# Optimization experiments

Hardware: AMD Instinct MI355X
Metric: run time of the kernel (lower is better)

## Reference

```python
import jax, jax.numpy as jnp
import numpy as np

N_NODES = 20000
N_EDGES = 640000
N_FEATS = 3703
HIDDEN = 50
N_CLASSES = 6
N_KENN_LAYERS = 3
# clause: not C_c(x) OR C_c(y) OR not Cite(x,y)  -> literal signs
SIGNS = np.array([-1.0, 1.0, -1.0], dtype=np.float32)


def setup_inputs() -> dict:
    key = jax.random.key(0)
    ks = jax.random.split(key, 12)
    features = jax.random.normal(ks[0], (N_NODES, N_FEATS), dtype=jnp.float32)
    relations = jax.random.normal(ks[1], (N_EDGES, 1), dtype=jnp.float32)
    sx = jax.random.randint(ks[2], (N_EDGES,), 0, N_NODES)
    sy = jax.random.randint(ks[3], (N_EDGES,), 0, N_NODES)

    def dense(k, fan_in, fan_out):
        return jax.random.normal(k, (fan_in, fan_out), dtype=jnp.float32) / np.sqrt(fan_in).astype(np.float32)

    W1 = dense(ks[4], N_FEATS, HIDDEN); b1 = jnp.zeros((HIDDEN,), jnp.float32)
    W2 = dense(ks[5], HIDDEN, HIDDEN);  b2 = jnp.zeros((HIDDEN,), jnp.float32)
    W3 = dense(ks[6], HIDDEN, HIDDEN);  b3 = jnp.zeros((HIDDEN,), jnp.float32)
    W4 = dense(ks[7], HIDDEN, N_CLASSES); b4 = jnp.zeros((N_CLASSES,), jnp.float32)
    # one learnable clause weight per class-clause, per KENN layer (init 0.5 as in KENN)
    clause_weights = jnp.full((N_KENN_LAYERS, N_CLASSES), 0.5, dtype=jnp.float32)
    return dict(features=features, relations=relations, sx=sx, sy=sy,
                W1=W1, b1=b1, W2=W2, b2=b2, W3=W3, b3=b3, W4=W4, b4=b4,
                clause_weights=clause_weights)


def _kenn_layer(z, relations, sx, sy, cw):
    # z: [N, C]; relations: [E, 1]; cw: [C] clause weights
    n = z.shape[0]
    zx = z[sx]                                   # [E, C] gather head literals
    zy = z[sy]                                   # [E, C] gather tail literals
    rel = jnp.broadcast_to(relations, (relations.shape[0], z.shape[1]))  # [E, C]
    signs = jnp.asarray(SIGNS)
    # signed literal preactivations per clause: [E, C, 3]
    v = jnp.stack([-zx, zy, -rel], axis=-1)
    # KENN boost: delta = w_c * softmax(signed preacts) * sign
    d = cw[None, :, None] * jax.nn.softmax(v, axis=-1) * signs[None, None, :]
    # scatter unary deltas back to nodes (relation delta is discarded)
    dz = jax.ops.segment_sum(d[..., 0], sx, num_segments=n)
    dz = dz + jax.ops.segment_sum(d[..., 1], sy, num_segments=n)
    return z + dz


def reference(features, relations, sx, sy, W1, b1, W2, b2, W3, b3, W4, b4, clause_weights):
    # MLP preactivations (dropout inactive at inference)
    x = jax.nn.relu(features @ W1 + b1)
    x = jax.nn.relu(x @ W2 + b2)
    x = jax.nn.relu(x @ W3 + b3)
    z = x @ W4 + b4                               # [N, 6]
    for i in range(N_KENN_LAYERS):
        z = _kenn_layer(z, relations, sx, sy, clause_weights[i])
    return jax.nn.softmax(z, axis=-1)
```

## Files before the change

kernel.cpp:

```cpp
#include <hip/hip_runtime.h>

#define M_NODES 20000
#define K_FEATS 3703
#define PADK 3712
#define NH 50
#define NC 6
#define N_EDGES_C 640000
#define NKB 116

typedef __attribute__((ext_vector_type(8))) __bf16 bf16x8;
typedef __attribute__((ext_vector_type(4))) float f32x4;

__global__ void k_packB(const float* __restrict__ W1, unsigned short* __restrict__ Bh,
                        unsigned short* __restrict__ Bl) {
  int idx = blockIdx.x * 256 + threadIdx.x;
  if (idx >= NKB * 4 * 64 * 8) return;
  int j = idx & 7;
  int lane = (idx >> 3) & 63;
  int t = (idx >> 9) & 3;
  int kb = idx >> 11;
  int k = kb * 32 + (lane >> 4) * 8 + j;
  int c = t * 16 + (lane & 15);
  float v = (k < K_FEATS && c < NH) ? W1[k * NH + c] : 0.f;
  __bf16 hb = (__bf16)v;
  float hf = (float)hb;
  __bf16 lb = (__bf16)(v - hf);
  Bh[idx] = *(unsigned short*)&hb;
  Bl[idx] = *(unsigned short*)&lb;
}

__global__ __launch_bounds__(256) void k_gemm1(const float* __restrict__ A,
    const unsigned short* __restrict__ Bph, const unsigned short* __restrict__ Bpl,
    float* __restrict__ part, int KS) {
  const int lane = threadIdx.x & 63;
  const int w = threadIdx.x >> 6;
  const int row0 = blockIdx.x * 128 + w * 32;
  const int s = blockIdx.y;
  const int ks = s * KS;
  const int ke = (ks + KS < PADK) ? ks + KS : PADK;
  const int nsteps = (ke - ks) >> 5;
  const int g = lane >> 4;
  const int rl = lane & 15;
  const int r0c = min(row0 + rl, M_NODES - 1);
  const int r1c = min(row0 + 16 + rl, M_NODES - 1);
  const float* a0p = A + (size_t)r0c * K_FEATS + 8 * g;
  const float* a1p = A + (size_t)r1c * K_FEATS + 8 * g;
  const bf16x8* BH = (const bf16x8*)Bph;
  const bf16x8* BL = (const bf16x8*)Bpl;

  f32x4 acc[2][4];
  #pragma unroll
  for (int i = 0; i < 2; ++i)
    #pragma unroll
    for (int t = 0; t < 4; ++t) acc[i][t] = (f32x4){0.f, 0.f, 0.f, 0.f};

  #define LOADA(d0, d1, k0) {                                     \
    d0[0] = *(const float4*)(a0p + (k0));                         \
    d0[1] = *(const float4*)(a0p + (k0) + 4);                     \
    d1[0] = *(const float4*)(a1p + (k0));                         \
    d1[1] = *(const float4*)(a1p + (k0) + 4); }
  #define LOADAG(d0, d1, k0) {                                    \
    _Pragma("unroll") for (int j = 0; j < 8; ++j) {               \
      int gk = (k0) + 8 * g + j;                                  \
      float v0 = (gk < K_FEATS) ? a0p[(k0) + j] : 0.f;            \
      float v1 = (gk < K_FEATS) ? a1p[(k0) + j] : 0.f;            \
      ((float*)d0)[j] = v0; ((float*)d1)[j] = v1; } }
  #define LDSEL(d0, d1, k0) {                                     \
    if ((k0) + 32 > K_FEATS) { LOADAG(d0, d1, k0) }               \
    else { LOADA(d0, d1, k0) } }

  #define BODY(sa0, sa1, k0) {                                    \
    const int kb4 = ((k0) >> 5) * 4;                              \
    bf16x8 bh0 = BH[(kb4 + 0) * 64 + lane];                       \
    bf16x8 bh1 = BH[(kb4 + 1) * 64 + lane];                       \
    bf16x8 bh2 = BH[(kb4 + 2) * 64 + lane];                       \
    bf16x8 bh3 = BH[(kb4 + 3) * 64 + lane];                       \
    bf16x8 bl0 = BL[(kb4 + 0) * 64 + lane];                       \
    bf16x8 bl1 = BL[(kb4 + 1) * 64 + lane];                       \
    bf16x8 bl2 = BL[(kb4 + 2) * 64 + lane];                       \
    bf16x8 bl3 = BL[(kb4 + 3) * 64 + lane];                       \
    bf16x8 ah0, al0, ah1, al1;                                    \
    _Pragma("unroll") for (int j = 0; j < 8; ++j) {               \
      float xv = ((const float*)sa0)[j];                          \
      __bf16 hb = (__bf16)xv; float hf = (float)hb;               \
      ah0[j] = hb; al0[j] = (__bf16)(xv - hf);                    \
      float yv = ((const float*)sa1)[j];                          \
      __bf16 hb2 = (__bf16)yv; float hf2 = (float)hb2;            \
      ah1[j] = hb2; al1[j] = (__bf16)(yv - hf2);                  \
    }                                                             \
    acc[0][0] = __builtin_amdgcn_mfma_f32_16x16x32_bf16(ah0, bh0, acc[0][0], 0, 0, 0); \
    acc[0][1] = __builtin_amdgcn_mfma_f32_16x16x32_bf16(ah0, bh1, acc[0][1], 0, 0, 0); \
    acc[0][2] = __builtin_amdgcn_mfma_f32_16x16x32_bf16(ah0, bh2, acc[0][2], 0, 0, 0); \
    acc[0][3] = __builtin_amdgcn_mfma_f32_16x16x32_bf16(ah0, bh3, acc[0][3], 0, 0, 0); \
    acc[1][0] = __builtin_amdgcn_mfma_f32_16x16x32_bf16(ah1, bh0, acc[1][0], 0, 0, 0); \
    acc[1][1] = __builtin_amdgcn_mfma_f32_16x16x32_bf16(ah1, bh1, acc[1][1], 0, 0, 0); \
    acc[1][2] = __builtin_amdgcn_mfma_f32_16x16x32_bf16(ah1, bh2, acc[1][2], 0, 0, 0); \
    acc[1][3] = __builtin_amdgcn_mfma_f32_16x16x32_bf16(ah1, bh3, acc[1][3], 0, 0, 0); \
    acc[0][0] = __builtin_amdgcn_mfma_f32_16x16x32_bf16(al0, bh0, acc[0][0], 0, 0, 0); \
    acc[0][1] = __builtin_amdgcn_mfma_f32_16x16x32_bf16(al0, bh1, acc[0][1], 0, 0, 0); \
    acc[0][2] = __builtin_amdgcn_mfma_f32_16x16x32_bf16(al0, bh2, acc[0][2], 0, 0, 0); \
    acc[0][3] = __builtin_amdgcn_mfma_f32_16x16x32_bf16(al0, bh3, acc[0][3], 0, 0, 0); \
    acc[1][0] = __builtin_amdgcn_mfma_f32_16x16x32_bf16(al1, bh0, acc[1][0], 0, 0, 0); \
    acc[1][1] = __builtin_amdgcn_mfma_f32_16x16x32_bf16(al1, bh1, acc[1][1], 0, 0, 0); \
    acc[1][2] = __builtin_amdgcn_mfma_f32_16x16x32_bf16(al1, bh2, acc[1][2], 0, 0, 0); \
    acc[1][3] = __builtin_amdgcn_mfma_f32_16x16x32_bf16(al1, bh3, acc[1][3], 0, 0, 0); \
    acc[0][0] = __builtin_amdgcn_mfma_f32_16x16x32_bf16(ah0, bl0, acc[0][0], 0, 0, 0); \
    acc[0][1] = __builtin_amdgcn_mfma_f32_16x16x32_bf16(ah0, bl1, acc[0][1], 0, 0, 0); \
    acc[0][2] = __builtin_amdgcn_mfma_f32_16x16x32_bf16(ah0, bl2, acc[0][2], 0, 0, 0); \
    acc[0][3] = __builtin_amdgcn_mfma_f32_16x16x32_bf16(ah0, bl3, acc[0][3], 0, 0, 0); \
    acc[1][0] = __builtin_amdgcn_mfma_f32_16x16x32_bf16(ah1, bl0, acc[1][0], 0, 0, 0); \
    acc[1][1] = __builtin_amdgcn_mfma_f32_16x16x32_bf16(ah1, bl1, acc[1][1], 0, 0, 0); \
    acc[1][2] = __builtin_amdgcn_mfma_f32_16x16x32_bf16(ah1, bl2, acc[1][2], 0, 0, 0); \
    acc[1][3] = __builtin_amdgcn_mfma_f32_16x16x32_bf16(ah1, bl3, acc[1][3], 0, 0, 0); }

  float4 p0a[2], p0b[2], p1a[2], p1b[2], p2a[2], p2b[2];
  LDSEL(p0a, p0b, ks);
  if (nsteps > 1) LDSEL(p1a, p1b, ks + 32);
  if (nsteps > 2) LDSEL(p2a, p2b, ks + 64);

  int t = 0;
  for (; t + 3 <= nsteps; t += 3) {
    const int k0 = ks + (t << 5);
    BODY(p0a, p0b, k0);
    if (t + 3 < nsteps) LDSEL(p0a, p0b, k0 + 96);
    BODY(p1a, p1b, k0 + 32);
    if (t + 4 < nsteps) LDSEL(p1a, p1b, k0 + 128);
    BODY(p2a, p2b, k0 + 64);
    if (t + 5 < nsteps) LDSEL(p2a, p2b, k0 + 160);
  }
  if (t < nsteps)     BODY(p0a, p0b, ks + (t << 5));
  if (t + 1 < nsteps) BODY(p1a, p1b, ks + ((t + 1) << 5));
  #undef LOADA
  #undef LOADAG
  #undef LDSEL
  #undef BODY

  float* p = part + (size_t)s * 1000000;
  #pragma unroll
  for (int i = 0; i < 2; ++i) {
    #pragma unroll
    for (int t2 = 0; t2 < 4; ++t2) {
      int col = t2 * 16 + rl;
      if (col < NH) {
        int rowb = row0 + i * 16 + g * 4;
        f32x4 v = acc[i][t2];
        #pragma unroll
        for (int q = 0; q < 4; ++q) {
          int row = rowb + q;
          if (row < M_NODES) p[row * NH + col] = v[q];
        }
      }
    }
  }
}

__global__ void k_epi(const float* __restrict__ part, const float* __restrict__ b1,
                      float* __restrict__ x1, int S) {
  int i = blockIdx.x * 256 + threadIdx.x;
  if (i >= M_NODES * NH) return;
  float v = b1[i % NH];
  for (int s = 0; s < S; ++s) v += part[(size_t)s * 1000000 + i];
  x1[i] = fmaxf(v, 0.f);
}

__global__ __launch_bounds__(256) void k_mlp(const float* __restrict__ x1,
    const float* __restrict__ W2, const float* __restrict__ b2,
    const float* __restrict__ W3, const float* __restrict__ b3,
    const float* __restrict__ W4, const float* __restrict__ b4,
    float* __restrict__ z) {
  __shared__ float lX[32 * 51];
  __shared__ float lW2[50 * 52];
  __shared__ float lW3[50 * 52];
  __shared__ float lW4[50 * 8];
  const int tid = threadIdx.x;
  const int row0 = blockIdx.x * 32;
  for (int idx = tid; idx < 2500; idx += 256) {
    int k = idx / 50, n = idx % 50;
    lW2[k * 52 + n] = W2[idx];
    lW3[k * 52 + n] = W3[idx];
  }
  for (int idx = tid; idx < 300; idx += 256) {
    int k = idx / 6, n = idx % 6;
    lW4[k * 8 + n] = W4[idx];
  }
  for (int idx = tid; idx < 1600; idx += 256) {
    int r = idx / 50, k = idx % 50;
    int gr = row0 + r;
    lX[r * 51 + k] = (gr < M_NODES) ? x1[gr * 50 + k] : 0.f;
  }
  __syncthreads();
  const int r = tid >> 3, cg = tid & 7;
  float x[50];
  #pragma unroll
  for (int k = 0; k < 50; ++k) x[k] = lX[r * 51 + k];

  for (int layer = 0; layer < 2; ++layer) {
    const float* lW = (layer == 0) ? lW2 : lW3;
    const float* bg = (layer == 0) ? b2 : b3;
    float acc[7];
    #pragma unroll
    for (int j = 0; j < 7; ++j) {
      int n = cg + 8 * j;
      acc[j] = (n < 50) ? bg[n] : 0.f;
    }
    #pragma unroll
    for (int k = 0; k < 50; ++k) {
      float xk = x[k];
      #pragma unroll
      for (int j = 0; j < 7; ++j) {
        int n = cg + 8 * j;
        if (n < 50) acc[j] = fmaf(xk, lW[k * 52 + n], acc[j]);
      }
    }
    __syncthreads();
    #pragma unroll
    for (int j = 0; j < 7; ++j) {
      int n = cg + 8 * j;
      if (n < 50) lX[r * 51 + n] = fmaxf(acc[j], 0.f);
    }
    __syncthreads();
    #pragma unroll
    for (int k = 0; k < 50; ++k) x[k] = lX[r * 51 + k];
  }
  if (cg < 6) {
    float accz = b4[cg];
    #pragma unroll
    for (int k = 0; k < 50; ++k) accz = fmaf(x[k], lW4[k * 8 + cg], accz);
    int gr = row0 + r;
    if (gr < M_NODES) z[gr * 6 + cg] = accz;
  }
}

__global__ void k_count(const int* __restrict__ sx, const int* __restrict__ sy,
                        int* __restrict__ cnt) {
  int e = blockIdx.x * 256 + threadIdx.x;
  if (e >= N_EDGES_C) return;
  atomicAdd(&cnt[sx[e]], 1);
  atomicAdd(&cnt[sy[e]], 1);
}

__global__ __launch_bounds__(1024) void k_scan(const int* __restrict__ cnt,
                                               int* __restrict__ off,
                                               int* __restrict__ cur) {
  __shared__ int sums[1024];
  int t = threadIdx.x;
  int base = t * 20;
  int local[20];
  int s = 0;
  #pragma unroll
  for (int j = 0; j < 20; ++j) {
    int idx = base + j;
    int v = (idx < M_NODES) ? cnt[idx] : 0;
    local[j] = s;
    s += v;
  }
  sums[t] = s;
  __syncthreads();
  for (int d = 1; d < 1024; d <<= 1) {
    int v = (t >= d) ? sums[t - d] : 0;
    __syncthreads();
    sums[t] += v;
    __syncthreads();
  }
  int excl = sums[t] - s;
  #pragma unroll
  for (int j = 0; j < 20; ++j) {
    int idx = base + j;
    if (idx < M_NODES) {
      int o = excl + local[j];
      off[idx] = o;
      cur[idx] = o;
    }
  }
  if (t == 1023) off[M_NODES] = sums[1023];
}

__global__ void k_scatter(const int* __restrict__ sx, const int* __restrict__ sy,
                          const float* __restrict__ rel,
                          int* __restrict__ cur, int2* __restrict__ ent) {
  int e = blockIdx.x * 256 + threadIdx.x;
  if (e >= N_EDGES_C) return;
  int a = sx[e], b = sy[e];
  int rb = __float_as_int(rel[e]);
  int p = atomicAdd(&cur[a], 1);
  ent[p] = make_int2((b << 1), rb);
  int q = atomicAdd(&cur[b], 1);
  ent[q] = make_int2((a << 1) | 1, rb);
}

__global__ __launch_bounds__(256) void k_gather(const float* __restrict__ z,
    const int* __restrict__ off, const int2* __restrict__ ent,
    const float* __restrict__ cw, float* __restrict__ zn,
    float* __restrict__ out, int last) {
  int t = blockIdx.x * 256 + threadIdx.x;
  int s = t & 7;
  int n = t >> 3;
  int o0 = off[n];
  int deg = off[n + 1] - o0;
  int lo = o0 + ((deg * s) >> 3);
  int hi = o0 + ((deg * (s + 1)) >> 3);

  const float2* zr = (const float2*)(z + n * 6);
  float2 a0 = zr[0], a1 = zr[1], a2 = zr[2];
  float znv[6] = {a0.x, a0.y, a1.x, a1.y, a2.x, a2.y};
  float w[6];
  #pragma unroll
  for (int c = 0; c < 6; ++c) w[c] = cw[c];
  float en_neg[6], en_pos[6];
  #pragma unroll
  for (int c = 0; c < 6; ++c) {
    en_neg[c] = __expf(-znv[c]);
    en_pos[c] = __expf(znv[c]);
  }
  float dz[6] = {0.f, 0.f, 0.f, 0.f, 0.f, 0.f};

  for (int i = lo; i < hi; ++i) {
    int2 e2 = ent[i];
    int partner = e2.x >> 1;
    int side = e2.x & 1;
    float r = __int_as_float(e2.y);
    const float2* zp2 = (const float2*)(z + partner * 6);
    float2 p0 = zp2[0], p1 = zp2[1], p2 = zp2[2];
    float zpv[6] = {p0.x, p0.y, p1.x, p1.y, p2.x, p2.y};
    float e2v = __expf(-r);
    #pragma unroll
    for (int c = 0; c < 6; ++c) {
      float e0 = side ? __expf(-zpv[c]) : en_neg[c];
      float e1 = side ? en_pos[c] : __expf(zpv[c]);
      float inv = w[c] / (e0 + e1 + e2v);
      dz[c] += (side ? e1 : -e0) * inv;
    }
  }

  #pragma unroll
  for (int c = 0; c < 6; ++c) {
    float v = dz[c];
    v += __shfl_xor(v, 1, 8);
    v += __shfl_xor(v, 2, 8);
    v += __shfl_xor(v, 4, 8);
    dz[c] = v;
  }

  if (s == 0) {
    float v[6];
    #pragma unroll
    for (int c = 0; c < 6; ++c) v[c] = znv[c] + dz[c];
    if (!last) {
      float2* o2 = (float2*)(zn + n * 6);
      o2[0] = make_float2(v[0], v[1]);
      o2[1] = make_float2(v[2], v[3]);
      o2[2] = make_float2(v[4], v[5]);
    } else {
      float m = v[0];
      #pragma unroll
      for (int c = 1; c < 6; ++c) m = fmaxf(m, v[c]);
      float sum = 0.f, ev[6];
      #pragma unroll
      for (int c = 0; c < 6; ++c) { ev[c] = __expf(v[c] - m); sum += ev[c]; }
      float inv = 1.f / sum;
      float2* o2 = (float2*)(out + n * 6);
      o2[0] = make_float2(ev[0] * inv, ev[1] * inv);
      o2[1] = make_float2(ev[2] * inv, ev[3] * inv);
      o2[2] = make_float2(ev[4] * inv, ev[5] * inv);
    }
  }
}

extern "C" void kernel_launch(void* const* d_in, const int* in_sizes, int n_in,
                              void* d_out, int out_size, void* d_ws, size_t ws_size,
                              hipStream_t stream) {
  const float* A   = (const float*)d_in[0];
  const float* rel = (const float*)d_in[1];
  const int*   sx  = (const int*)d_in[2];
  const int*   sy  = (const int*)d_in[3];
  const float* W1  = (const float*)d_in[4];
  const float* b1  = (const float*)d_in[5];
  const float* W2  = (const float*)d_in[6];
  const float* b2  = (const float*)d_in[7];
  const float* W3  = (const float*)d_in[8];
  const float* b3  = (const float*)d_in[9];
  const float* W4  = (const float*)d_in[10];
  const float* b4  = (const float*)d_in[11];
  const float* cw  = (const float*)d_in[12];

  const int S = 8, KS = 512;

  float* base = (float*)d_ws;
  float* part = base;
  float* x1   = base + 8000000;
  float* zA   = base + 9000000;
  float* zB   = base + 9120000;
  unsigned short* Bph = (unsigned short*)(base + 9240000);
  unsigned short* Bpl = (unsigned short*)(base + 9360000);

  int*  cnt  = (int*)base;
  int*  off  = (int*)base + 24576;
  int*  cur  = (int*)base + 49152;
  int2* ent  = (int2*)((int*)base + 73728);

  k_packB<<<(NKB * 4 * 64 * 8 + 255) / 256, 256, 0, stream>>>(W1, Bph, Bpl);
  k_gemm1<<<dim3(157, S), 256, 0, stream>>>(A, Bph, Bpl, part, KS);
  k_epi<<<(M_NODES * NH + 255) / 256, 256, 0, stream>>>(part, b1, x1, S);
  k_mlp<<<(M_NODES + 31) / 32, 256, 0, stream>>>(x1, W2, b2, W3, b3, W4, b4, zA);

  hipMemsetAsync(cnt, 0, (M_NODES + 1) * sizeof(int), stream);
  k_count<<<(N_EDGES_C + 255) / 256, 256, 0, stream>>>(sx, sy, cnt);
  k_scan<<<1, 1024, 0, stream>>>(cnt, off, cur);
  k_scatter<<<(N_EDGES_C + 255) / 256, 256, 0, stream>>>(sx, sy, rel, cur, ent);

  float* zc = zA;
  float* zn = zB;
  for (int l = 0; l < 3; ++l) {
    k_gather<<<M_NODES * 8 / 256, 256, 0, stream>>>(
        zc, off, ent, cw + 6 * l, zn, (float*)d_out, (l == 2) ? 1 : 0);
    float* t = zc; zc = zn; zn = t;
  }
}
```

Measured before the change: 346.3 us.

## Halve per-wave row tile in GEMM1 and shorten the A prefetch pipeline

Each wave in the first GEMM now computes a 16-row tile instead of 32 rows, and the grid doubles from 157 to 313 row blocks. The triple-buffered A prefetch becomes a simpler two-stage double buffer. The aim is to cut register pressure and add waves, so the memory-bound feature-matrix stream hides latency better. In exchange, each packed W1 fragment loaded from cache now serves half as many rows, which doubles B-operand load traffic per output.

```diff
diff --git a/kernel.cpp b/kernel.cpp
--- a/kernel.cpp
+++ b/kernel.cpp
@@ -34,7 +34,7 @@
     float* __restrict__ part, int KS) {
   const int lane = threadIdx.x & 63;
   const int w = threadIdx.x >> 6;
-  const int row0 = blockIdx.x * 128 + w * 32;
+  const int row0 = blockIdx.x * 64 + w * 16;
   const int s = blockIdx.y;
   const int ks = s * KS;
   const int ke = (ks + KS < PADK) ? ks + KS : PADK;
@@ -42,34 +42,26 @@
   const int g = lane >> 4;
   const int rl = lane & 15;
   const int r0c = min(row0 + rl, M_NODES - 1);
-  const int r1c = min(row0 + 16 + rl, M_NODES - 1);
   const float* a0p = A + (size_t)r0c * K_FEATS + 8 * g;
-  const float* a1p = A + (size_t)r1c * K_FEATS + 8 * g;
   const bf16x8* BH = (const bf16x8*)Bph;
   const bf16x8* BL = (const bf16x8*)Bpl;
 
-  f32x4 acc[2][4];
-  #pragma unroll
-  for (int i = 0; i < 2; ++i)
-    #pragma unroll
-    for (int t = 0; t < 4; ++t) acc[i][t] = (f32x4){0.f, 0.f, 0.f, 0.f};
-
-  #define LOADA(d0, d1, k0) {                                     \
+  f32x4 acc[4];
+  #pragma unroll
+  for (int t = 0; t < 4; ++t) acc[t] = (f32x4){0.f, 0.f, 0.f, 0.f};
+
+  #define LOADA(d0, k0) {                                         \
     d0[0] = *(const float4*)(a0p + (k0));                         \
-    d0[1] = *(const float4*)(a0p + (k0) + 4);                     \
-    d1[0] = *(const float4*)(a1p + (k0));                         \
-    d1[1] = *(const float4*)(a1p + (k0) + 4); }
-  #define LOADAG(d0, d1, k0) {                                    \
+    d0[1] = *(const float4*)(a0p + (k0) + 4); }
+  #define LOADAG(d0, k0) {                                        \
     _Pragma("unroll") for (int j = 0; j < 8; ++j) {               \
       int gk = (k0) + 8 * g + j;                                  \
-      float v0 = (gk < K_FEATS) ? a0p[(k0) + j] : 0.f;            \
-      float v1 = (gk < K_FEATS) ? a1p[(k0) + j] : 0.f;            \
-      ((float*)d0)[j] = v0; ((float*)d1)[j] = v1; } }
-  #define LDSEL(d0, d1, k0) {                                     \
-    if ((k0) + 32 > K_FEATS) { LOADAG(d0, d1, k0) }               \
-    else { LOADA(d0, d1, k0) } }
-
-  #define BODY(sa0, sa1, k0) {                                    \
+      ((float*)d0)[j] = (gk < K_FEATS) ? a0p[(k0) + j] : 0.f; } }
+  #define LDSEL(d0, k0) {                                         \
+    if ((k0) + 32 > K_FEATS) { LOADAG(d0, k0) }                   \
+    else { LOADA(d0, k0) } }
+
+  #define BODY(sa, k0) {                                          \
     const int kb4 = ((k0) >> 5) * 4;                              \
     bf16x8 bh0 = BH[(kb4 + 0) * 64 + lane];                       \
     bf16x8 bh1 = BH[(kb4 + 1) * 64 + lane];                       \
@@ -79,57 +71,37 @@
     bf16x8 bl1 = BL[(kb4 + 1) * 64 + lane];                       \
     bf16x8 bl2 = BL[(kb4 + 2) * 64 + lane];                       \
     bf16x8 bl3 = BL[(kb4 + 3) * 64 + lane];                       \
-    bf16x8 ah0, al0, ah1, al1;                                    \
+    bf16x8 ah, al;                                                \
     _Pragma("unroll") for (int j = 0; j < 8; ++j) {               \
-      float xv = ((const float*)sa0)[j];                          \
+      float xv = ((const float*)sa)[j];                           \
       __bf16 hb = (__bf16)xv; float hf = (float)hb;               \
-      ah0[j] = hb; al0[j] = (__bf16)(xv - hf);                    \
-      float yv = ((const float*)sa1)[j];                          \
-      __bf16 hb2 = (__bf16)yv; float hf2 = (float)hb2;            \
-      ah1[j] = hb2; al1[j] = (__bf16)(yv - hf2);                  \
+      ah[j] = hb; al[j] = (__bf16)(xv - hf);                      \
     }                                                             \
-    acc[0][0] = __builtin_amdgcn_mfma_f32_16x16x32_bf16(ah0, bh0, acc[0][0], 0, 0, 0); \
-    acc[0][1] = __builtin_amdgcn_mfma_f32_16x16x32_bf16(ah0, bh1, acc[0][1], 0, 0, 0); \
-    acc[0][2] = __builtin_amdgcn_mfma_f32_16x16x32_bf16(ah0, bh2, acc[0][2], 0, 0, 0); \
-    acc[0][3] = __builtin_amdgcn_mfma_f32_16x16x32_bf16(ah0, bh3, acc[0][3], 0, 0, 0); \
-    acc[1][0] = __builtin_amdgcn_mfma_f32_16x16x32_bf16(ah1, bh0, acc[1][0], 0, 0, 0); \
-    acc[1][1] = __builtin_amdgcn_mfma_f32_16x16x32_bf16(ah1, bh1, acc[1][1], 0, 0, 0); \
-    acc[1][2] = __builtin_amdgcn_mfma_f32_16x16x32_bf16(ah1, bh2, acc[1][2], 0, 0, 0); \
-    acc[1][3] = __builtin_amdgcn_mfma_f32_16x16x32_bf16(ah1, bh3, acc[1][3], 0, 0, 0); \
-    acc[0][0] = __builtin_amdgcn_mfma_f32_16x16x32_bf16(al0, bh0, acc[0][0], 0, 0, 0); \
-    acc[0][1] = __builtin_amdgcn_mfma_f32_16x16x32_bf16(al0, bh1, acc[0][1], 0, 0, 0); \
-    acc[0][2] = __builtin_amdgcn_mfma_f32_16x16x32_bf16(al0, bh2, acc[0][2], 0, 0, 0); \
-    acc[0][3] = __builtin_amdgcn_mfma_f32_16x16x32_bf16(al0, bh3, acc[0][3], 0, 0, 0); \
-    acc[1][0] = __builtin_amdgcn_mfma_f32_16x16x32_bf16(al1, bh0, acc[1][0], 0, 0, 0); \
-    acc[1][1] = __builtin_amdgcn_mfma_f32_16x16x32_bf16(al1, bh1, acc[1][1], 0, 0, 0); \
-    acc[1][2] = __builtin_amdgcn_mfma_f32_16x16x32_bf16(al1, bh2, acc[1][2], 0, 0, 0); \
-    acc[1][3] = __builtin_amdgcn_mfma_f32_16x16x32_bf16(al1, bh3, acc[1][3], 0, 0, 0); \
-    acc[0][0] = __builtin_amdgcn_mfma_f32_16x16x32_bf16(ah0, bl0, acc[0][0], 0, 0, 0); \
-    acc[0][1] = __builtin_amdgcn_mfma_f32_16x16x32_bf16(ah0, bl1, acc[0][1], 0, 0, 0); \
-    acc[0][2] = __builtin_amdgcn_mfma_f32_16x16x32_bf16(ah0, bl2, acc[0][2], 0, 0, 0); \
-    acc[0][3] = __builtin_amdgcn_mfma_f32_16x16x32_bf16(ah0, bl3, acc[0][3], 0, 0, 0); \
-    acc[1][0] = __builtin_amdgcn_mfma_f32_16x16x32_bf16(ah1, bl0, acc[1][0], 0, 0, 0); \
-    acc[1][1] = __builtin_amdgcn_mfma_f32_16x16x32_bf16(ah1, bl1, acc[1][1], 0, 0, 0); \
-    acc[1][2] = __builtin_amdgcn_mfma_f32_16x16x32_bf16(ah1, bl2, acc[1][2], 0, 0, 0); \
-    acc[1][3] = __builtin_amdgcn_mfma_f32_16x16x32_bf16(ah1, bl3, acc[1][3], 0, 0, 0); }
-
-  float4 p0a[2], p0b[2], p1a[2], p1b[2], p2a[2], p2b[2];
-  LDSEL(p0a, p0b, ks);
-  if (nsteps > 1) LDSEL(p1a, p1b, ks + 32);
-  if (nsteps > 2) LDSEL(p2a, p2b, ks + 64);
-
-  int t = 0;
-  for (; t + 3 <= nsteps; t += 3) {
-    const int k0 = ks + (t << 5);
-    BODY(p0a, p0b, k0);
-    if (t + 3 < nsteps) LDSEL(p0a, p0b, k0 + 96);
-    BODY(p1a, p1b, k0 + 32);
-    if (t + 4 < nsteps) LDSEL(p1a, p1b, k0 + 128);
-    BODY(p2a, p2b, k0 + 64);
-    if (t + 5 < nsteps) LDSEL(p2a, p2b, k0 + 160);
-  }
-  if (t < nsteps)     BODY(p0a, p0b, ks + (t << 5));
-  if (t + 1 < nsteps) BODY(p1a, p1b, ks + ((t + 1) << 5));
+    acc[0] = __builtin_amdgcn_mfma_f32_16x16x32_bf16(ah, bh0, acc[0], 0, 0, 0); \
+    acc[1] = __builtin_amdgcn_mfma_f32_16x16x32_bf16(ah, bh1, acc[1], 0, 0, 0); \
+    acc[2] = __builtin_amdgcn_mfma_f32_16x16x32_bf16(ah, bh2, acc[2], 0, 0, 0); \
+    acc[3] = __builtin_amdgcn_mfma_f32_16x16x32_bf16(ah, bh3, acc[3], 0, 0, 0); \
+    acc[0] = __builtin_amdgcn_mfma_f32_16x16x32_bf16(al, bh0, acc[0], 0, 0, 0); \
+    acc[1] = __builtin_amdgcn_mfma_f32_16x16x32_bf16(al, bh1, acc[1], 0, 0, 0); \
+    acc[2] = __builtin_amdgcn_mfma_f32_16x16x32_bf16(al, bh2, acc[2], 0, 0, 0); \
+    acc[3] = __builtin_amdgcn_mfma_f32_16x16x32_bf16(al, bh3, acc[3], 0, 0, 0); \
+    acc[0] = __builtin_amdgcn_mfma_f32_16x16x32_bf16(ah, bl0, acc[0], 0, 0, 0); \
+    acc[1] = __builtin_amdgcn_mfma_f32_16x16x32_bf16(ah, bl1, acc[1], 0, 0, 0); \
+    acc[2] = __builtin_amdgcn_mfma_f32_16x16x32_bf16(ah, bl2, acc[2], 0, 0, 0); \
+    acc[3] = __builtin_amdgcn_mfma_f32_16x16x32_bf16(ah, bl3, acc[3], 0, 0, 0); }
+
+  float4 xa[2], ya[2];
+  LOADA(xa, ks);
+  for (int t2 = 0; t2 < nsteps; t2 += 2) {
+    const int k0 = ks + (t2 << 5);
+    const int k1 = k0 + 32;
+    LDSEL(ya, k1);
+    BODY(xa, k0);
+    if (t2 + 2 < nsteps) {
+      LDSEL(xa, k0 + 64);
+    }
+    BODY(ya, k1);
+  }
   #undef LOADA
   #undef LOADAG
   #undef LDSEL
@@ -137,18 +109,15 @@
 
   float* p = part + (size_t)s * 1000000;
   #pragma unroll
-  for (int i = 0; i < 2; ++i) {
-    #pragma unroll
-    for (int t2 = 0; t2 < 4; ++t2) {
-      int col = t2 * 16 + rl;
-      if (col < NH) {
-        int rowb = row0 + i * 16 + g * 4;
-        f32x4 v = acc[i][t2];
-        #pragma unroll
-        for (int q = 0; q < 4; ++q) {
-          int row = rowb + q;
-          if (row < M_NODES) p[row * NH + col] = v[q];
-        }
+  for (int t2 = 0; t2 < 4; ++t2) {
+    int col = t2 * 16 + rl;
+    if (col < NH) {
+      int rowb = row0 + g * 4;
+      f32x4 v = acc[t2];
+      #pragma unroll
+      for (int q = 0; q < 4; ++q) {
+        int row = rowb + q;
+        if (row < M_NODES) p[row * NH + col] = v[q];
       }
     }
   }
@@ -399,7 +368,7 @@
   int2* ent  = (int2*)((int*)base + 73728);
 
   k_packB<<<(NKB * 4 * 64 * 8 + 255) / 256, 256, 0, stream>>>(W1, Bph, Bpl);
-  k_gemm1<<<dim3(157, S), 256, 0, stream>>>(A, Bph, Bpl, part, KS);
+  k_gemm1<<<dim3(313, S), 256, 0, stream>>>(A, Bph, Bpl, part, KS);
   k_epi<<<(M_NODES * NH + 255) / 256, 256, 0, stream>>>(part, b1, x1, S);
   k_mlp<<<(M_NODES + 31) / 32, 256, 0, stream>>>(x1, W2, b2, W3, b3, W4, b4, zA);
 
```

Measured after the change: 360.4 us. 4.0% more time.

## Fuse CSR-build stages into MLP pipeline kernels via block-range dispatch

Applied to the files above, without the earlier changes.

Merges the edge-count pass into the weight-packing kernel, the prefix scan into the GEMM epilogue kernel, and the edge scatter into the small-MLP kernel. Each pair is selected by block index, which cuts the launch count from eight to four plus the memset. It also lets the independent CSR graph work run alongside the dense stages. The workspace layout moves so the CSR buffers no longer alias the GEMM partials. The scan now runs as a single 256-thread block with serial 79-element chunks, which may be slower than the previous 1024-thread scan.

```diff
diff --git a/kernel.cpp b/kernel.cpp
--- a/kernel.cpp
+++ b/kernel.cpp
@@ -7,26 +7,37 @@
 #define NC 6
 #define N_EDGES_C 640000
 #define NKB 116
+#define PACK_BLOCKS 928
+#define EDGE_BLOCKS 2500
+#define MLP_BLOCKS 625
 
 typedef __attribute__((ext_vector_type(8))) __bf16 bf16x8;
 typedef __attribute__((ext_vector_type(4))) float f32x4;
 
-__global__ void k_packB(const float* __restrict__ W1, unsigned short* __restrict__ Bh,
-                        unsigned short* __restrict__ Bl) {
-  int idx = blockIdx.x * 256 + threadIdx.x;
-  if (idx >= NKB * 4 * 64 * 8) return;
-  int j = idx & 7;
-  int lane = (idx >> 3) & 63;
-  int t = (idx >> 9) & 3;
-  int kb = idx >> 11;
-  int k = kb * 32 + (lane >> 4) * 8 + j;
-  int c = t * 16 + (lane & 15);
-  float v = (k < K_FEATS && c < NH) ? W1[k * NH + c] : 0.f;
-  __bf16 hb = (__bf16)v;
-  float hf = (float)hb;
-  __bf16 lb = (__bf16)(v - hf);
-  Bh[idx] = *(unsigned short*)&hb;
-  Bl[idx] = *(unsigned short*)&lb;
+__global__ __launch_bounds__(256) void k_pack_count(const float* __restrict__ W1,
+    unsigned short* __restrict__ Bh, unsigned short* __restrict__ Bl,
+    const int* __restrict__ sx, const int* __restrict__ sy, int* __restrict__ cnt) {
+  if (blockIdx.x < PACK_BLOCKS) {
+    int idx = blockIdx.x * 256 + threadIdx.x;
+    if (idx >= NKB * 4 * 64 * 8) return;
+    int j = idx & 7;
+    int lane = (idx >> 3) & 63;
+    int t = (idx >> 9) & 3;
+    int kb = idx >> 11;
+    int k = kb * 32 + (lane >> 4) * 8 + j;
+    int c = t * 16 + (lane & 15);
+    float v = (k < K_FEATS && c < NH) ? W1[k * NH + c] : 0.f;
+    __bf16 hb = (__bf16)v;
+    float hf = (float)hb;
+    __bf16 lb = (__bf16)(v - hf);
+    Bh[idx] = *(unsigned short*)&hb;
+    Bl[idx] = *(unsigned short*)&lb;
+  } else {
+    int e = (blockIdx.x - PACK_BLOCKS) * 256 + threadIdx.x;
+    if (e >= N_EDGES_C) return;
+    atomicAdd(&cnt[sx[e]], 1);
+    atomicAdd(&cnt[sy[e]], 1);
+  }
 }
 
 __global__ __launch_bounds__(256) void k_gemm1(const float* __restrict__ A,
@@ -154,24 +165,62 @@
   }
 }
 
-__global__ void k_epi(const float* __restrict__ part, const float* __restrict__ b1,
-                      float* __restrict__ x1, int S) {
-  int i = blockIdx.x * 256 + threadIdx.x;
-  if (i >= M_NODES * NH) return;
-  float v = b1[i % NH];
-  for (int s = 0; s < S; ++s) v += part[(size_t)s * 1000000 + i];
-  x1[i] = fmaxf(v, 0.f);
-}
-
-__global__ __launch_bounds__(256) void k_mlp(const float* __restrict__ x1,
+__global__ __launch_bounds__(256) void k_epi_scan(const float* __restrict__ part,
+    const float* __restrict__ b1, float* __restrict__ x1, int S,
+    const int* __restrict__ cnt, int* __restrict__ off, int* __restrict__ cur) {
+  __shared__ int sums[256];
+  if (blockIdx.x == 0) {
+    int t = threadIdx.x;
+    int lo = t * 79;
+    int hi = lo + 79; if (hi > M_NODES) hi = M_NODES;
+    int s = 0;
+    for (int i = lo; i < hi; ++i) s += cnt[i];
+    sums[t] = s;
+    __syncthreads();
+    for (int d = 1; d < 256; d <<= 1) {
+      int v = (t >= d) ? sums[t - d] : 0;
+      __syncthreads();
+      sums[t] += v;
+      __syncthreads();
+    }
+    int run = sums[t] - s;
+    for (int i = lo; i < hi; ++i) {
+      off[i] = run;
+      cur[i] = run;
+      run += cnt[i];
+    }
+    if (t == 255) off[M_NODES] = sums[255];
+  } else {
+    int i = (blockIdx.x - 1) * 256 + threadIdx.x;
+    if (i >= M_NODES * NH) return;
+    float v = b1[i % NH];
+    for (int s = 0; s < S; ++s) v += part[(size_t)s * 1000000 + i];
+    x1[i] = fmaxf(v, 0.f);
+  }
+}
+
+__global__ __launch_bounds__(256) void k_mlp_scatter(const float* __restrict__ x1,
     const float* __restrict__ W2, const float* __restrict__ b2,
     const float* __restrict__ W3, const float* __restrict__ b3,
     const float* __restrict__ W4, const float* __restrict__ b4,
-    float* __restrict__ z) {
+    float* __restrict__ z,
+    const int* __restrict__ sx, const int* __restrict__ sy,
+    const float* __restrict__ rel, int* __restrict__ cur, int2* __restrict__ ent) {
   __shared__ float lX[32 * 51];
   __shared__ float lW2[50 * 52];
   __shared__ float lW3[50 * 52];
   __shared__ float lW4[50 * 8];
+  if (blockIdx.x >= MLP_BLOCKS) {
+    int e = (blockIdx.x - MLP_BLOCKS) * 256 + threadIdx.x;
+    if (e >= N_EDGES_C) return;
+    int a = sx[e], b = sy[e];
+    int rb = __float_as_int(rel[e]);
+    int p = atomicAdd(&cur[a], 1);
+    ent[p] = make_int2((b << 1), rb);
+    int q = atomicAdd(&cur[b], 1);
+    ent[q] = make_int2((a << 1) | 1, rb);
+    return;
+  }
   const int tid = threadIdx.x;
   const int row0 = blockIdx.x * 32;
   for (int idx = tid; idx < 2500; idx += 256) {
@@ -229,63 +278,6 @@
     int gr = row0 + r;
     if (gr < M_NODES) z[gr * 6 + cg] = accz;
   }
-}
-
-__global__ void k_count(const int* __restrict__ sx, const int* __restrict__ sy,
-                        int* __restrict__ cnt) {
-  int e = blockIdx.x * 256 + threadIdx.x;
-  if (e >= N_EDGES_C) return;
-  atomicAdd(&cnt[sx[e]], 1);
-  atomicAdd(&cnt[sy[e]], 1);
-}
-
-__global__ __launch_bounds__(1024) void k_scan(const int* __restrict__ cnt,
-                                               int* __restrict__ off,
-                                               int* __restrict__ cur) {
-  __shared__ int sums[1024];
-  int t = threadIdx.x;
-  int base = t * 20;
-  int local[20];
-  int s = 0;
-  #pragma unroll
-  for (int j = 0; j < 20; ++j) {
-    int idx = base + j;
-    int v = (idx < M_NODES) ? cnt[idx] : 0;
-    local[j] = s;
-    s += v;
-  }
-  sums[t] = s;
-  __syncthreads();
-  for (int d = 1; d < 1024; d <<= 1) {
-    int v = (t >= d) ? sums[t - d] : 0;
-    __syncthreads();
-    sums[t] += v;
-    __syncthreads();
-  }
-  int excl = sums[t] - s;
-  #pragma unroll
-  for (int j = 0; j < 20; ++j) {
-    int idx = base + j;
-    if (idx < M_NODES) {
-      int o = excl + local[j];
-      off[idx] = o;
-      cur[idx] = o;
-    }
-  }
-  if (t == 1023) off[M_NODES] = sums[1023];
-}
-
-__global__ void k_scatter(const int* __restrict__ sx, const int* __restrict__ sy,
-                          const float* __restrict__ rel,
-                          int* __restrict__ cur, int2* __restrict__ ent) {
-  int e = blockIdx.x * 256 + threadIdx.x;
-  if (e >= N_EDGES_C) return;
-  int a = sx[e], b = sy[e];
-  int rb = __float_as_int(rel[e]);
-  int p = atomicAdd(&cur[a], 1);
-  ent[p] = make_int2((b << 1), rb);
-  int q = atomicAdd(&cur[b], 1);
-  ent[q] = make_int2((a << 1) | 1, rb);
 }
 
 __global__ __launch_bounds__(256) void k_gather(const float* __restrict__ z,
@@ -392,21 +384,17 @@
   float* zB   = base + 9120000;
   unsigned short* Bph = (unsigned short*)(base + 9240000);
   unsigned short* Bpl = (unsigned short*)(base + 9360000);
-
-  int*  cnt  = (int*)base;
-  int*  off  = (int*)base + 24576;
-  int*  cur  = (int*)base + 49152;
-  int2* ent  = (int2*)((int*)base + 73728);
-
-  k_packB<<<(NKB * 4 * 64 * 8 + 255) / 256, 256, 0, stream>>>(W1, Bph, Bpl);
+  int*  cnt  = (int*)(base + 9480000);
+  int*  off  = (int*)(base + 9504000);
+  int*  cur  = (int*)(base + 9528000);
+  int2* ent  = (int2*)(base + 9552000);
+
+  hipMemsetAsync(cnt, 0, (M_NODES + 1) * sizeof(int), stream);
+  k_pack_count<<<PACK_BLOCKS + EDGE_BLOCKS, 256, 0, stream>>>(W1, Bph, Bpl, sx, sy, cnt);
   k_gemm1<<<dim3(157, S), 256, 0, stream>>>(A, Bph, Bpl, part, KS);
-  k_epi<<<(M_NODES * NH + 255) / 256, 256, 0, stream>>>(part, b1, x1, S);
-  k_mlp<<<(M_NODES + 31) / 32, 256, 0, stream>>>(x1, W2, b2, W3, b3, W4, b4, zA);
-
-  hipMemsetAsync(cnt, 0, (M_NODES + 1) * sizeof(int), stream);
-  k_count<<<(N_EDGES_C + 255) / 256, 256, 0, stream>>>(sx, sy, cnt);
-  k_scan<<<1, 1024, 0, stream>>>(cnt, off, cur);
-  k_scatter<<<(N_EDGES_C + 255) / 256, 256, 0, stream>>>(sx, sy, rel, cur, ent);
+  k_epi_scan<<<1 + (M_NODES * NH + 255) / 256, 256, 0, stream>>>(part, b1, x1, S, cnt, off, cur);
+  k_mlp_scatter<<<MLP_BLOCKS + EDGE_BLOCKS, 256, 0, stream>>>(
+      x1, W2, b2, W3, b3, W4, b4, zA, sx, sy, rel, cur, ent);
 
   float* zc = zA;
   float* zn = zB;
```

Measured after the change: 376.7 us. +8.8%, slower.
